# Kernel optimization log

Hardware: AMD Instinct MI355X
Metric: run time of the kernel (lower is better)

The kernel has to match this reference:

```python
import jax, jax.numpy as jnp
import numpy as np

Ng, Np, B, T = 4096, 512, 128, 100

def setup_inputs() -> dict:
    key = jax.random.key(0)
    ks = jax.random.split(key, 6)
    # xavier-ish scaling for the learned weights
    def xavier(k, shape):
        fan_in, fan_out = shape[1], shape[0]
        lim = jnp.sqrt(6.0 / (fan_in + fan_out))
        return jax.random.uniform(k, shape, jnp.float32, -lim, lim)
    return {
        "v": jax.random.normal(ks[0], (B, T, 2), jnp.float32),
        "p0": jax.random.uniform(ks[1], (B, Np), jnp.float32),
        "W_enc": xavier(ks[2], (Ng, Np)),   # init_position_encoder.weight
        "W_ih": xavier(ks[3], (Ng, 2)),     # RNN weight_ih_l0
        "W_hh": xavier(ks[4], (Ng, Ng)),    # RNN weight_hh_l0
        "W_dec": xavier(ks[5], (Np, Ng)),   # decoder.weight
    }

def reference(v, p0, W_enc, W_ih, W_hh, W_dec):
    # h0 = init_position_encoder(p0): (B, Ng)
    h0 = p0 @ W_enc.T
    # precompute input projections for all steps: (T, B, Ng)
    vin = jnp.einsum('btk,gk->tbg', v, W_ih)

    def step(h, x):
        h_new = jax.nn.relu(x + h @ W_hh.T)  # (B, Ng)
        return h_new, h_new

    _, hs = jax.lax.scan(step, h0, vin)      # hs: (T, B, Ng)
    g = jnp.swapaxes(hs, 0, 1)               # (B, T, Ng)
    preds = g @ W_dec.T                      # (B, T, Np)
    return jax.nn.log_softmax(preds, axis=-1)
```

## Files before the change

kernel.cpp:

```cpp
#include <hip/hip_runtime.h>

#define NG 4096
#define NP 512
#define BSZ 128
#define NT 100
#define KS 16
#define KBLK 256
#define KC 64

typedef _Float16 f16;
typedef __attribute__((ext_vector_type(8))) _Float16 half8;
typedef __attribute__((ext_vector_type(4))) _Float16 half4v;
typedef __attribute__((ext_vector_type(16))) float f32x16;

__device__ inline f32x16 mfma16(half8 a, half8 b, f32x16 c) {
  return __builtin_amdgcn_mfma_f32_32x32x16_f16(a, b, c, 0, 0, 0);
}
__device__ __forceinline__ void gload16(const void* g, void* l) {
  __builtin_amdgcn_global_load_lds(
      (const __attribute__((address_space(1))) void*)g,
      (__attribute__((address_space(3))) void*)l, 16, 0, 0);
}

__global__ __launch_bounds__(256) void conv_f16(
    const float* __restrict__ src, f16* __restrict__ dst, int n4)
{
  int i = blockIdx.x * 256 + threadIdx.x;
  if (i >= n4) return;
  const float4 x = ((const float4*)src)[i];
  half4v h = { (f16)x.x, (f16)x.y, (f16)x.z, (f16)x.w };
  *(half4v*)&dst[(size_t)i * 4] = h;
}

__global__ __launch_bounds__(256) void encode_kernel(
    const float* __restrict__ p0, const float* __restrict__ wenc,
    f16* __restrict__ h0)
{
  __shared__ float sp[NP];
  const int b = blockIdx.y;
  const int g = blockIdx.x * 256 + threadIdx.x;
  for (int i = threadIdx.x; i < NP; i += 256) sp[i] = p0[(size_t)b * NP + i];
  __syncthreads();
  const float4* wr = (const float4*)(wenc + (size_t)g * NP);
  float acc = 0.f;
  #pragma unroll 8
  for (int p4 = 0; p4 < NP / 4; ++p4) {
    float4 ww = wr[p4];
    acc += ww.x * sp[4*p4] + ww.y * sp[4*p4+1] + ww.z * sp[4*p4+2] + ww.w * sp[4*p4+3];
  }
  h0[(size_t)b * NG + g] = (f16)acc;
}

__global__ __launch_bounds__(256, 2) void step_gemm(
    const f16* __restrict__ whh16, const f16* __restrict__ hprev,
    f16* __restrict__ part)
{
  __shared__ __align__(128) char lds[2 * 32768];
  const int tid = threadIdx.x;
  const int w = tid >> 6, lane = tid & 63;
  const int wm = w & 1, wn = w >> 1;
  const int l31 = lane & 31, hi = lane >> 5;
  const int n0 = blockIdx.y * 128;
  const int k0 = blockIdx.x * KBLK;

  const int lrow8 = lane >> 3;
  const int swz = ((lane & 7) ^ lrow8) * 16;
  const char* gA = (const char*)hprev;
  const char* gB = (const char*)(whh16 + (size_t)n0 * NG);

  f32x16 acc[2][2] = {};

  auto stage = [&](int buf, int c) {
    const size_t kb = (size_t)((k0 + c * KC) * 2) + swz;
    char* lb = lds + buf * 32768;
    #pragma unroll
    for (int j = 0; j < 4; ++j) {
      const int r = w * 32 + j * 8;
      gload16(gA + (size_t)(r + lrow8) * (NG * 2) + kb, lb + r * 128);
      gload16(gB + (size_t)(r + lrow8) * (NG * 2) + kb, lb + 16384 + r * 128);
    }
  };
  auto compute = [&](int buf) {
    const char* bA = lds + buf * 32768;
    const char* bB = bA + 16384;
    const int swr = (lane & 7) << 4;
    #pragma unroll
    for (int kk = 0; kk < 4; ++kk) {
      const int bc = (kk * 32 + (hi << 4)) ^ swr;
      half8 a0 = *(const half8*)(bA + (wm * 64 + l31) * 128 + bc);
      half8 a1 = *(const half8*)(bA + (wm * 64 + 32 + l31) * 128 + bc);
      half8 b0 = *(const half8*)(bB + (wn * 64 + l31) * 128 + bc);
      half8 b1 = *(const half8*)(bB + (wn * 64 + 32 + l31) * 128 + bc);
      acc[0][0] = mfma16(a0, b0, acc[0][0]);
      acc[0][1] = mfma16(a0, b1, acc[0][1]);
      acc[1][0] = mfma16(a1, b0, acc[1][0]);
      acc[1][1] = mfma16(a1, b1, acc[1][1]);
    }
  };

  stage(0, 0);
  __syncthreads();
  #pragma unroll 1
  for (int c = 0; c < 4; ++c) {
    if (c < 3) stage((c + 1) & 1, c + 1);
    compute(c & 1);
    __syncthreads();
  }

  f16* po = part + (size_t)blockIdx.x * (BSZ * NG);
  #pragma unroll
  for (int mf = 0; mf < 2; ++mf) {
    #pragma unroll
    for (int q = 0; q < 16; ++q) {
      const int row = wm * 64 + mf * 32 + (q & 3) + 8 * (q >> 2) + 4 * hi;
      #pragma unroll
      for (int nf = 0; nf < 2; ++nf) {
        const int col = n0 + wn * 64 + nf * 32 + l31;
        po[(size_t)row * NG + col] = (f16)acc[mf][nf][q];
      }
    }
  }
}

__global__ __launch_bounds__(256) void step_reduce(
    const f16* __restrict__ part, const float* __restrict__ v,
    const float* __restrict__ wih, f16* __restrict__ hout, int t)
{
  const int i = blockIdx.x * 256 + threadIdx.x;
  const int b = i >> 9;
  const int gi = (i & 511) * 8;
  const half8* p = (const half8*)part + (((size_t)b * NG + gi) >> 3);
  float s[8];
  half8 q0 = p[0];
  #pragma unroll
  for (int j = 0; j < 8; ++j) s[j] = (float)q0[j];
  #pragma unroll
  for (int k = 1; k < KS; ++k) {
    half8 q = p[(size_t)k * (BSZ * NG / 8)];
    #pragma unroll
    for (int j = 0; j < 8; ++j) s[j] += (float)q[j];
  }
  const float2 vb = *(const float2*)&v[((size_t)b * NT + t) * 2];
  const float4* wr = (const float4*)(wih + (size_t)gi * 2);
  half8 h;
  #pragma unroll
  for (int j2 = 0; j2 < 4; ++j2) {
    const float4 ww = wr[j2];
    const float x0 = fmaxf(s[j2 * 2]     + vb.x * ww.x + vb.y * ww.y, 0.f);
    const float x1 = fmaxf(s[j2 * 2 + 1] + vb.x * ww.z + vb.y * ww.w, 0.f);
    h[j2 * 2]     = (f16)x0;
    h[j2 * 2 + 1] = (f16)x1;
  }
  *(half8*)&hout[(size_t)b * NG + gi] = h;
}

__global__ __launch_bounds__(512, 2) void decode_kernel(
    const f16* __restrict__ hs, const f16* __restrict__ wdec16,
    float* __restrict__ out)
{
  __shared__ __align__(128) char lds[2 * 73728];
  __shared__ float redm[8][64];
  __shared__ float reds[8][64];
  __shared__ float gLS[64];
  const int tid = threadIdx.x;
  const int w = tid >> 6, lane = tid & 63;
  const int l31 = lane & 31, hi = lane >> 5;
  const int r0 = blockIdx.x * 64;

  const int lrow8 = lane >> 3;
  const int swz = ((lane & 7) ^ lrow8) * 16;
  const char* gA = (const char*)(hs + (size_t)r0 * NG);
  const char* gB = (const char*)wdec16;

  f32x16 acc[2][2] = {};

  auto stage = [&](int buf, int c) {
    const size_t kb = (size_t)(c * 128) + swz;
    char* lb = lds + buf * 73728;
    gload16(gA + (size_t)(w * 8 + lrow8) * (NG * 2) + kb, lb + w * 1024);
    #pragma unroll
    for (int j = 0; j < 8; ++j) {
      const int r = w * 64 + j * 8;
      gload16(gB + (size_t)(r + lrow8) * (NG * 2) + kb, lb + 8192 + r * 128);
    }
  };
  auto compute = [&](int buf) {
    const char* bA = lds + buf * 73728;
    const char* bB = bA + 8192;
    const int swr = (lane & 7) << 4;
    #pragma unroll
    for (int kk = 0; kk < 4; ++kk) {
      const int bc = (kk * 32 + (hi << 4)) ^ swr;
      half8 a0 = *(const half8*)(bA + l31 * 128 + bc);
      half8 a1 = *(const half8*)(bA + (32 + l31) * 128 + bc);
      half8 b0 = *(const half8*)(bB + (w * 64 + l31) * 128 + bc);
      half8 b1 = *(const half8*)(bB + (w * 64 + 32 + l31) * 128 + bc);
      acc[0][0] = mfma16(a0, b0, acc[0][0]);
      acc[0][1] = mfma16(a0, b1, acc[0][1]);
      acc[1][0] = mfma16(a1, b0, acc[1][0]);
      acc[1][1] = mfma16(a1, b1, acc[1][1]);
    }
  };

  stage(0, 0);
  __syncthreads();
  #pragma unroll 1
  for (int c = 0; c < 64; ++c) {
    if (c < 63) stage((c + 1) & 1, c + 1);
    compute(c & 1);
    __syncthreads();
  }

  #pragma unroll
  for (int mf = 0; mf < 2; ++mf) {
    #pragma unroll
    for (int q = 0; q < 16; ++q) {
      float m = fmaxf(acc[mf][0][q], acc[mf][1][q]);
      #pragma unroll
      for (int d = 1; d < 32; d <<= 1) m = fmaxf(m, __shfl_xor(m, d));
      if (l31 == q) redm[w][mf * 32 + (q & 3) + 8 * (q >> 2) + 4 * hi] = m;
    }
  }
  __syncthreads();
  if (tid < 64) {
    float M = redm[0][tid];
    #pragma unroll
    for (int ww = 1; ww < 8; ++ww) M = fmaxf(M, redm[ww][tid]);
    gLS[tid] = M;
  }
  __syncthreads();
  #pragma unroll
  for (int mf = 0; mf < 2; ++mf) {
    #pragma unroll
    for (int q = 0; q < 16; ++q) {
      const int rl = mf * 32 + (q & 3) + 8 * (q >> 2) + 4 * hi;
      const float M = gLS[rl];
      float e = __expf(acc[mf][0][q] - M) + __expf(acc[mf][1][q] - M);
      #pragma unroll
      for (int d = 1; d < 32; d <<= 1) e += __shfl_xor(e, d);
      if (l31 == q) reds[w][rl] = e;
    }
  }
  __syncthreads();
  if (tid < 64) {
    float S = reds[0][tid];
    #pragma unroll
    for (int ww = 1; ww < 8; ++ww) S += reds[ww][tid];
    gLS[tid] = gLS[tid] + __logf(S);
  }
  __syncthreads();
  #pragma unroll
  for (int mf = 0; mf < 2; ++mf) {
    #pragma unroll
    for (int q = 0; q < 16; ++q) {
      const int rl = mf * 32 + (q & 3) + 8 * (q >> 2) + 4 * hi;
      const int r = r0 + rl;
      const int tt = r >> 7, b = r & 127;
      const float lg = gLS[rl];
      float* orow = out + ((size_t)b * NT + tt) * NP + w * 64 + l31;
      orow[0]  = acc[mf][0][q] - lg;
      orow[32] = acc[mf][1][q] - lg;
    }
  }
}


extern "C" void kernel_launch(void* const* d_in, const int* in_sizes, int n_in,
                              void* d_out, int out_size, void* d_ws, size_t ws_size,
                              hipStream_t stream)
{
  const float* v    = (const float*)d_in[0];
  const float* p0   = (const float*)d_in[1];
  const float* wenc = (const float*)d_in[2];
  const float* wih  = (const float*)d_in[3];
  const float* whh  = (const float*)d_in[4];
  const float* wdec = (const float*)d_in[5];
  float* out = (float*)d_out;
  char* ws = (char*)d_ws;

  f16* whh16  = (f16*)(ws);
  f16* wdec16 = (f16*)(ws + 33554432);
  f16* h016   = (f16*)(ws + 37748736);
  f16* hs     = (f16*)(ws + 38797312);
  f16* part   = (f16*)d_out;
  const size_t BNG = (size_t)BSZ * NG;

  conv_f16<<<dim3(16384), dim3(256), 0, stream>>>(whh, whh16, 4194304);
  conv_f16<<<dim3(2048), dim3(256), 0, stream>>>(wdec, wdec16, 524288);
  encode_kernel<<<dim3(16, 128), dim3(256), 0, stream>>>(p0, wenc, h016);

  for (int t = 0; t < NT; ++t) {
    const f16* hp = (t == 0) ? h016 : hs + (size_t)(t - 1) * BNG;
    step_gemm<<<dim3(KS, 32), dim3(256), 0, stream>>>(whh16, hp, part);
    step_reduce<<<dim3(256), dim3(256), 0, stream>>>(part, v, wih, hs + (size_t)t * BNG, t);
  }
  decode_kernel<<<dim3(200), dim3(512), 0, stream>>>(hs, wdec16, out);
}
```

Measured before the change: 1.679 ms.

## Use 512-thread in-block k-split GEMM to halve partial sums per step

```diff
diff --git a/kernel.cpp b/kernel.cpp
--- a/kernel.cpp
+++ b/kernel.cpp
@@ -4,9 +4,6 @@
 #define NP 512
 #define BSZ 128
 #define NT 100
-#define KS 16
-#define KBLK 256
-#define KC 64
 
 typedef _Float16 f16;
 typedef __attribute__((ext_vector_type(8))) _Float16 half8;
@@ -32,52 +29,33 @@
   *(half4v*)&dst[(size_t)i * 4] = h;
 }
 
-__global__ __launch_bounds__(256) void encode_kernel(
-    const float* __restrict__ p0, const float* __restrict__ wenc,
-    f16* __restrict__ h0)
-{
-  __shared__ float sp[NP];
-  const int b = blockIdx.y;
-  const int g = blockIdx.x * 256 + threadIdx.x;
-  for (int i = threadIdx.x; i < NP; i += 256) sp[i] = p0[(size_t)b * NP + i];
-  __syncthreads();
-  const float4* wr = (const float4*)(wenc + (size_t)g * NP);
-  float acc = 0.f;
-  #pragma unroll 8
-  for (int p4 = 0; p4 < NP / 4; ++p4) {
-    float4 ww = wr[p4];
-    acc += ww.x * sp[4*p4] + ww.y * sp[4*p4+1] + ww.z * sp[4*p4+2] + ww.w * sp[4*p4+3];
-  }
-  h0[(size_t)b * NG + g] = (f16)acc;
-}
-
-__global__ __launch_bounds__(256, 2) void step_gemm(
-    const f16* __restrict__ whh16, const f16* __restrict__ hprev,
-    f16* __restrict__ part)
-{
-  __shared__ __align__(128) char lds[2 * 32768];
+__global__ __launch_bounds__(512, 1) void gemm_ksplit(
+    const f16* __restrict__ bmat, const f16* __restrict__ amat,
+    f16* __restrict__ part, int krow, int kblk, int nch)
+{
+  __shared__ __align__(128) char lds[98304];
   const int tid = threadIdx.x;
   const int w = tid >> 6, lane = tid & 63;
-  const int wm = w & 1, wn = w >> 1;
+  const int g = w >> 2, s = w & 3, wm = s & 1, wn = s >> 1;
   const int l31 = lane & 31, hi = lane >> 5;
   const int n0 = blockIdx.y * 128;
-  const int k0 = blockIdx.x * KBLK;
-
-  const int lrow8 = lane >> 3;
-  const int swz = ((lane & 7) ^ lrow8) * 16;
-  const char* gA = (const char*)hprev;
-  const char* gB = (const char*)(whh16 + (size_t)n0 * NG);
+  const size_t krb = (size_t)krow * 2;
+
+  const int lrow = lane >> 3, lu = lane & 7;
+  const int sw = (lu ^ lrow) * 16;
+  const char* gA = (const char*)amat;
+  const char* gB = (const char*)bmat + (size_t)n0 * krb;
 
   f32x16 acc[2][2] = {};
 
   auto stage = [&](int buf, int c) {
-    const size_t kb = (size_t)((k0 + c * KC) * 2) + swz;
+    const size_t kb = (size_t)((blockIdx.x * kblk + c * 64) * 2) + sw;
     char* lb = lds + buf * 32768;
     #pragma unroll
-    for (int j = 0; j < 4; ++j) {
-      const int r = w * 32 + j * 8;
-      gload16(gA + (size_t)(r + lrow8) * (NG * 2) + kb, lb + r * 128);
-      gload16(gB + (size_t)(r + lrow8) * (NG * 2) + kb, lb + 16384 + r * 128);
+    for (int i = 0; i < 2; ++i) {
+      const int r = w * 8 + i * 64;
+      gload16(gA + (size_t)(r + lrow) * krb + kb, lb + r * 128);
+      gload16(gB + (size_t)(r + lrow) * krb + kb, lb + 16384 + r * 128);
     }
   };
   auto compute = [&](int buf) {
@@ -85,8 +63,8 @@
     const char* bB = bA + 16384;
     const int swr = (lane & 7) << 4;
     #pragma unroll
-    for (int kk = 0; kk < 4; ++kk) {
-      const int bc = (kk * 32 + (hi << 4)) ^ swr;
+    for (int kk = 0; kk < 2; ++kk) {
+      const int bc = (g * 64 + kk * 32 + (hi << 4)) ^ swr;
       half8 a0 = *(const half8*)(bA + (wm * 64 + l31) * 128 + bc);
       half8 a1 = *(const half8*)(bA + (wm * 64 + 32 + l31) * 128 + bc);
       half8 b0 = *(const half8*)(bB + (wn * 64 + l31) * 128 + bc);
@@ -101,30 +79,53 @@
   stage(0, 0);
   __syncthreads();
   #pragma unroll 1
-  for (int c = 0; c < 4; ++c) {
-    if (c < 3) stage((c + 1) & 1, c + 1);
+  for (int c = 0; c < nch; ++c) {
+    if (c + 1 < nch) stage((c + 1) & 1, c + 1);
     compute(c & 1);
     __syncthreads();
   }
 
-  f16* po = part + (size_t)blockIdx.x * (BSZ * NG);
-  #pragma unroll
-  for (int mf = 0; mf < 2; ++mf) {
-    #pragma unroll
-    for (int q = 0; q < 16; ++q) {
-      const int row = wm * 64 + mf * 32 + (q & 3) + 8 * (q >> 2) + 4 * hi;
+  float* ex = (float*)lds;
+  f16* exh = (f16*)(lds + 65536);
+  if (g == 1) {
+    #pragma unroll
+    for (int mf = 0; mf < 2; ++mf)
       #pragma unroll
-      for (int nf = 0; nf < 2; ++nf) {
-        const int col = n0 + wn * 64 + nf * 32 + l31;
-        po[(size_t)row * NG + col] = (f16)acc[mf][nf][q];
-      }
-    }
-  }
-}
-
-__global__ __launch_bounds__(256) void step_reduce(
+      for (int nf = 0; nf < 2; ++nf)
+        #pragma unroll
+        for (int q = 0; q < 16; ++q) {
+          const int row = wm * 64 + mf * 32 + (q & 3) + 8 * (q >> 2) + 4 * hi;
+          const int col = wn * 64 + nf * 32 + l31;
+          ex[row * 128 + col] = acc[mf][nf][q];
+        }
+  }
+  __syncthreads();
+  if (g == 0) {
+    #pragma unroll
+    for (int mf = 0; mf < 2; ++mf)
+      #pragma unroll
+      for (int nf = 0; nf < 2; ++nf)
+        #pragma unroll
+        for (int q = 0; q < 16; ++q) {
+          const int row = wm * 64 + mf * 32 + (q & 3) + 8 * (q >> 2) + 4 * hi;
+          const int col = wn * 64 + nf * 32 + l31;
+          exh[row * 128 + col] = (f16)(acc[mf][nf][q] + ex[row * 128 + col]);
+        }
+  }
+  __syncthreads();
+  f16* po = part + (size_t)blockIdx.x * (BSZ * NG) + n0;
+  const int ur = tid >> 4, uu = tid & 15;
+  #pragma unroll
+  for (int i = 0; i < 4; ++i) {
+    const int r = i * 32 + ur;
+    *(half8*)(po + (size_t)r * NG + uu * 8) = *(const half8*)(exh + r * 128 + uu * 8);
+  }
+}
+
+__global__ __launch_bounds__(256) void reduce_kernel(
     const f16* __restrict__ part, const float* __restrict__ v,
-    const float* __restrict__ wih, f16* __restrict__ hout, int t)
+    const float* __restrict__ wih, f16* __restrict__ hout,
+    int t, int nsets, int dobias)
 {
   const int i = blockIdx.x * 256 + threadIdx.x;
   const int b = i >> 9;
@@ -134,22 +135,25 @@
   half8 q0 = p[0];
   #pragma unroll
   for (int j = 0; j < 8; ++j) s[j] = (float)q0[j];
-  #pragma unroll
-  for (int k = 1; k < KS; ++k) {
+  #pragma unroll 1
+  for (int k = 1; k < nsets; ++k) {
     half8 q = p[(size_t)k * (BSZ * NG / 8)];
     #pragma unroll
     for (int j = 0; j < 8; ++j) s[j] += (float)q[j];
   }
-  const float2 vb = *(const float2*)&v[((size_t)b * NT + t) * 2];
-  const float4* wr = (const float4*)(wih + (size_t)gi * 2);
   half8 h;
-  #pragma unroll
-  for (int j2 = 0; j2 < 4; ++j2) {
-    const float4 ww = wr[j2];
-    const float x0 = fmaxf(s[j2 * 2]     + vb.x * ww.x + vb.y * ww.y, 0.f);
-    const float x1 = fmaxf(s[j2 * 2 + 1] + vb.x * ww.z + vb.y * ww.w, 0.f);
-    h[j2 * 2]     = (f16)x0;
-    h[j2 * 2 + 1] = (f16)x1;
+  if (dobias) {
+    const float2 vb = *(const float2*)&v[((size_t)b * NT + t) * 2];
+    const float4* wr = (const float4*)(wih + (size_t)gi * 2);
+    #pragma unroll
+    for (int j2 = 0; j2 < 4; ++j2) {
+      const float4 ww = wr[j2];
+      h[j2 * 2]     = (f16)fmaxf(s[j2 * 2]     + vb.x * ww.x + vb.y * ww.y, 0.f);
+      h[j2 * 2 + 1] = (f16)fmaxf(s[j2 * 2 + 1] + vb.x * ww.z + vb.y * ww.w, 0.f);
+    }
+  } else {
+    #pragma unroll
+    for (int j = 0; j < 8; ++j) h[j] = (f16)s[j];
   }
   *(half8*)&hout[(size_t)b * NG + gi] = h;
 }
@@ -281,18 +285,24 @@
   f16* whh16  = (f16*)(ws);
   f16* wdec16 = (f16*)(ws + 33554432);
   f16* h016   = (f16*)(ws + 37748736);
-  f16* hs     = (f16*)(ws + 38797312);
+  f16* p016   = (f16*)(ws + 38797312);
+  f16* hs     = (f16*)(ws + 38928384);
   f16* part   = (f16*)d_out;
   const size_t BNG = (size_t)BSZ * NG;
 
   conv_f16<<<dim3(16384), dim3(256), 0, stream>>>(whh, whh16, 4194304);
   conv_f16<<<dim3(2048), dim3(256), 0, stream>>>(wdec, wdec16, 524288);
-  encode_kernel<<<dim3(16, 128), dim3(256), 0, stream>>>(p0, wenc, h016);
+  conv_f16<<<dim3(64), dim3(256), 0, stream>>>(p0, p016, 16384);
+  conv_f16<<<dim3(4096), dim3(256), 0, stream>>>(wenc, (f16*)(ws + 143785984), 524288);
+  f16* wenc16 = (f16*)(ws + 143785984);
+
+  gemm_ksplit<<<dim3(2, 32), dim3(512), 0, stream>>>(wenc16, p016, part, NP, 256, 4);
+  reduce_kernel<<<dim3(256), dim3(256), 0, stream>>>(part, v, wih, h016, 0, 2, 0);
 
   for (int t = 0; t < NT; ++t) {
     const f16* hp = (t == 0) ? h016 : hs + (size_t)(t - 1) * BNG;
-    step_gemm<<<dim3(KS, 32), dim3(256), 0, stream>>>(whh16, hp, part);
-    step_reduce<<<dim3(256), dim3(256), 0, stream>>>(part, v, wih, hs + (size_t)t * BNG, t);
+    gemm_ksplit<<<dim3(8, 32), dim3(512), 0, stream>>>(whh16, hp, part, NG, 512, 8);
+    reduce_kernel<<<dim3(256), dim3(256), 0, stream>>>(part, v, wih, hs + (size_t)t * BNG, t, 8, 1);
   }
   decode_kernel<<<dim3(200), dim3(512), 0, stream>>>(hs, wdec16, out);
 }
```

After: 1.741 ms. 3.7% more time.
